# Optimization experiments

Hardware: AMD Instinct MI355X
Metric: run time of the kernel (lower is better)

The kernel has to match this reference:

```python
import jax, jax.numpy as jnp
import numpy as np

B, NW, WS, FD = 16, 256, 8, 96
D = WS * WS * FD        # 6144 flattened window dim
MID = 512               # expert hidden dim
NE = 16                 # num experts


def setup_inputs() -> dict:
    key = jax.random.key(0)
    ks = jax.random.split(key, 7)
    s1 = 1.0 / np.sqrt(D)
    s2 = 1.0 / np.sqrt(MID)
    x = jax.random.normal(ks[0], (B, NW, WS, WS, FD), dtype=jnp.float32)
    # stacked expert weights (torch Linear: y = x @ W.T + b)
    w1 = jax.random.uniform(ks[1], (NE, D, MID), jnp.float32, -s1, s1)
    b1 = jax.random.uniform(ks[2], (NE, MID), jnp.float32, -s1, s1)
    w2 = jax.random.uniform(ks[3], (NE, MID), jnp.float32, -s2, s2)  # out dim 1, squeezed
    b2 = jax.random.uniform(ks[4], (NE,), jnp.float32, -s2, s2)
    gw = jax.random.uniform(ks[5], (D, NE), jnp.float32, -s1, s1)
    gb = jax.random.uniform(ks[6], (NE,), jnp.float32, -s1, s1)
    return {"x": x, "w1": w1, "b1": b1, "w2": w2, "b2": b2, "gw": gw, "gb": gb}


def reference(x, w1, b1, w2, b2, gw, gb):
    bsz, nw = x.shape[0], x.shape[1]
    xf = x.reshape(bsz * nw, D)                          # [T, D]
    h = jax.nn.relu(jnp.einsum('td,ndm->tnm', xf, w1) + b1)  # [T, N, MID]
    e = jnp.einsum('tnm,nm->tn', h, w2) + b2             # [T, N] expert scalar outputs
    g = jax.nn.softmax(xf @ gw + gb, axis=-1)            # [T, N] gating
    out = jax.nn.sigmoid(jnp.sum(g * e, axis=-1))        # [T]
    return out.reshape(bsz, nw)
```

## Files before the change

### kernel.cpp

```cpp
#include <hip/hip_runtime.h>
#include <hip/hip_bf16.h>
#include <stdint.h>

#define T_TOK 4096
#define DD    6144
#define MIDD  512
#define NEXP  16

typedef __attribute__((ext_vector_type(8))) __bf16 bf16x8;
typedef __attribute__((ext_vector_type(4))) float  f32x4;

__device__ __forceinline__ unsigned short f2bf(float f) {
  unsigned int u = __builtin_bit_cast(unsigned int, f);
  u += 0x7fffu + ((u >> 16) & 1u);
  return (unsigned short)(u >> 16);
}

__device__ __forceinline__ void gload16(const void* g, void* l) {
  __builtin_amdgcn_global_load_lds((__attribute__((address_space(1))) void*)g,
                                   (__attribute__((address_space(3))) void*)l,
                                   16, 0, 0);
}

__global__ __launch_bounds__(256) void k_cvt_x(const float4* __restrict__ x,
                                               ushort4* __restrict__ xb, int n4) {
  int i = blockIdx.x * blockDim.x + threadIdx.x;
  const int stride = gridDim.x * blockDim.x;
  for (; i < n4; i += stride) {
    const float4 v = x[i];
    ushort4 o;
    o.x = f2bf(v.x); o.y = f2bf(v.y); o.z = f2bf(v.z); o.w = f2bf(v.w);
    xb[i] = o;
  }
}

__global__ __launch_bounds__(256) void k_trc_w1(const float* __restrict__ w1,
                                                unsigned short* __restrict__ w1t) {
  __shared__ float tile[32][33];
  const int n  = blockIdx.z;
  const int d0 = blockIdx.y * 32;
  const int m0 = blockIdx.x * 32;
  const int r  = threadIdx.x >> 3;
  const int c4 = threadIdx.x & 7;

  const float4 v = *(const float4*)(w1 + (size_t)n * DD * MIDD +
                                    (size_t)(d0 + r) * MIDD + m0 + c4 * 4);
  tile[r][c4 * 4 + 0] = v.x;
  tile[r][c4 * 4 + 1] = v.y;
  tile[r][c4 * 4 + 2] = v.z;
  tile[r][c4 * 4 + 3] = v.w;
  __syncthreads();
  ushort4 o;
  o.x = f2bf(tile[c4 * 4 + 0][r]);
  o.y = f2bf(tile[c4 * 4 + 1][r]);
  o.z = f2bf(tile[c4 * 4 + 2][r]);
  o.w = f2bf(tile[c4 * 4 + 3][r]);
  *(ushort4*)(w1t + (size_t)n * MIDD * DD + (size_t)(m0 + r) * DD + d0 + c4 * 4) = o;
}

__global__ __launch_bounds__(256) void k_gemm(const unsigned short* __restrict__ Xb,
                                              const unsigned short* __restrict__ W1T,
                                              const float* __restrict__ b1,
                                              const float* __restrict__ w2,
                                              float* __restrict__ e_part) {
  __shared__ char lds[16384];
  char* ldsA = lds;
  char* ldsB = lds + 8192;

  const int tid  = threadIdx.x;
  const int wid  = tid >> 6;
  const int lane = tid & 63;
  const int bn   = blockIdx.x;
  const int bm   = blockIdx.y;
  const int row0 = bm * 128;
  const int col0 = bn * 128;
  const int ne   = col0 >> 9;
  const int m0   = col0 & 511;
  const int wr = wid >> 1, wc = wid & 1;
  const int kb = lane >> 4, lr = lane & 15;

  f32x4 acc[4][4] = {};

  const unsigned short* Ag = Xb + (size_t)row0 * DD + wid * 8;
  const unsigned short* Bg = W1T + ((size_t)ne * MIDD + m0) * DD + wid * 8;
  char* ldsAw = ldsA + wid * 2048;
  char* ldsBw = ldsB + wid * 2048;

  for (int k0 = 0; k0 < DD; k0 += 32) {
    __syncthreads();
    gload16(Ag + (size_t)lane        * DD + k0, ldsAw);
    gload16(Ag + (size_t)(64 + lane) * DD + k0, ldsAw + 1024);
    gload16(Bg + (size_t)lane        * DD + k0, ldsBw);
    gload16(Bg + (size_t)(64 + lane) * DD + k0, ldsBw + 1024);
    __syncthreads();

    bf16x8 af[4], bfr[4];
#pragma unroll
    for (int m = 0; m < 4; ++m)
      af[m] = *(const bf16x8*)(ldsA + kb * 2048 + (wr * 64 + m * 16 + lr) * 16);
#pragma unroll
    for (int nn = 0; nn < 4; ++nn)
      bfr[nn] = *(const bf16x8*)(ldsB + kb * 2048 + (wc * 64 + nn * 16 + lr) * 16);
#pragma unroll
    for (int m = 0; m < 4; ++m)
#pragma unroll
      for (int nn = 0; nn < 4; ++nn)
        acc[m][nn] = __builtin_amdgcn_mfma_f32_16x16x32_bf16(af[m], bfr[nn],
                                                             acc[m][nn], 0, 0, 0);
  }

  const int part = ((bn & 3) << 1) | wc;
  float b1v[4], w2v[4];
#pragma unroll
  for (int bj = 0; bj < 4; ++bj) {
    const int mcol = m0 + wc * 64 + bj * 16 + lr;
    b1v[bj] = b1[ne * MIDD + mcol];
    w2v[bj] = w2[ne * MIDD + mcol];
  }
#pragma unroll
  for (int ai = 0; ai < 4; ++ai) {
#pragma unroll
    for (int i = 0; i < 4; ++i) {
      float s = 0.f;
#pragma unroll
      for (int bj = 0; bj < 4; ++bj) {
        float h = acc[ai][bj][i] + b1v[bj];
        h = fmaxf(h, 0.f);
        s += h * w2v[bj];
      }
      s += __shfl_xor(s, 1);
      s += __shfl_xor(s, 2);
      s += __shfl_xor(s, 4);
      s += __shfl_xor(s, 8);
      if (lr == 0) {
        const int row = row0 + wr * 64 + ai * 16 + kb * 4 + i;
        e_part[((size_t)row * NEXP + ne) * 8 + part] = s;
      }
    }
  }
}

__global__ __launch_bounds__(256) void k_gate(const float* __restrict__ x,
                                              const float* __restrict__ gw,
                                              float* __restrict__ l_part) {
  const int tl = threadIdx.x >> 2, ng = threadIdx.x & 3;
  const int tg = blockIdx.x >> 3, ds = blockIdx.x & 7;
  const int t  = tg * 64 + tl;
  const float* xp  = x  + (size_t)t * DD + ds * 768;
  const float* gwp = gw + (size_t)(ds * 768) * NEXP + ng * 4;
  float a[4] = {0.f, 0.f, 0.f, 0.f};
  for (int c = 0; c < 768; c += 4) {
    const float4 xv = *(const float4*)(xp + c);
    const float xs[4] = {xv.x, xv.y, xv.z, xv.w};
#pragma unroll
    for (int j = 0; j < 4; ++j) {
      const float4 g4 = *(const float4*)(gwp + (size_t)(c + j) * NEXP);
      a[0] += xs[j] * g4.x; a[1] += xs[j] * g4.y;
      a[2] += xs[j] * g4.z; a[3] += xs[j] * g4.w;
    }
  }
  float* lp = l_part + ((size_t)t * NEXP + ng * 4) * 8 + ds;
  lp[0] = a[0]; lp[8] = a[1]; lp[16] = a[2]; lp[24] = a[3];
}

__global__ __launch_bounds__(256) void k_combine(const float* __restrict__ l_part,
                                                 const float* __restrict__ e_part,
                                                 const float* __restrict__ gb,
                                                 const float* __restrict__ b2,
                                                 float* __restrict__ out) {
  const int tl = threadIdx.x >> 4, n = threadIdx.x & 15;
  const int t  = blockIdx.x * 16 + tl;
  const float4* lp = (const float4*)(l_part + ((size_t)t * NEXP + n) * 8);
  const float4 l0 = lp[0], l1 = lp[1];
  const float logit = l0.x + l0.y + l0.z + l0.w + l1.x + l1.y + l1.z + l1.w + gb[n];
  const float4* ep = (const float4*)(e_part + ((size_t)t * NEXP + n) * 8);
  const float4 e0 = ep[0], e1 = ep[1];
  const float ev = e0.x + e0.y + e0.z + e0.w + e1.x + e1.y + e1.z + e1.w + b2[n];
  float m = logit;
  m = fmaxf(m, __shfl_xor(m, 1));
  m = fmaxf(m, __shfl_xor(m, 2));
  m = fmaxf(m, __shfl_xor(m, 4));
  m = fmaxf(m, __shfl_xor(m, 8));
  const float p = __expf(logit - m);
  float pe = p * ev, pz = p;
  pe += __shfl_xor(pe, 1); pz += __shfl_xor(pz, 1);
  pe += __shfl_xor(pe, 2); pz += __shfl_xor(pz, 2);
  pe += __shfl_xor(pe, 4); pz += __shfl_xor(pz, 4);
  pe += __shfl_xor(pe, 8); pz += __shfl_xor(pz, 8);
  if (n == 0) {
    const float z = pe / pz;
    out[t] = 1.f / (1.f + __expf(-z));
  }
}

extern "C" void kernel_launch(void* const* d_in, const int* in_sizes, int n_in,
                              void* d_out, int out_size, void* d_ws, size_t ws_size,
                              hipStream_t stream) {
  const float* x  = (const float*)d_in[0];
  const float* w1 = (const float*)d_in[1];
  const float* b1 = (const float*)d_in[2];
  const float* w2 = (const float*)d_in[3];
  const float* b2 = (const float*)d_in[4];
  const float* gw = (const float*)d_in[5];
  const float* gb = (const float*)d_in[6];
  float* out = (float*)d_out;

  char* ws = (char*)d_ws;
  unsigned short* Xb  = (unsigned short*)ws;
  unsigned short* W1T = (unsigned short*)(ws + 50331648);
  float* e_part = (float*)(ws + 150994944);
  float* l_part = (float*)(ws + 153092096);

  k_cvt_x<<<2048, 256, 0, stream>>>((const float4*)x, (ushort4*)Xb, (T_TOK * DD) / 4);
  k_trc_w1<<<dim3(MIDD / 32, DD / 32, NEXP), 256, 0, stream>>>(w1, W1T);
  k_gemm<<<dim3(64, 32), 256, 0, stream>>>(Xb, W1T, b1, w2, e_part);
  k_gate<<<512, 256, 0, stream>>>(x, gw, l_part);
  k_combine<<<256, 256, 0, stream>>>(l_part, e_part, gb, b2, out);
}
```

Measured before the change: 1.227 ms.

## Double-buffer GEMM LDS loads, remap blocks for XCD locality, widen w1 transpose tiles

The GEMM now double-buffers its A/B tiles in LDS, issuing the next k-slice's global-to-LDS loads before the current slice's MFMAs, which cuts one barrier per iteration. The grid becomes 1D with an index remap that interleaves blocks (blockIdx&7 shifted high) so blocks likely co-resident on the same chiplet share row/column tiles in cache. The w1 transpose kernel moves to 64x64 tiles with 16-byte stores to improve write coalescing. The cost is doubled LDS per block (32 KB), which may lower occupancy, and a more complex block mapping.

```diff
diff --git a/kernel.cpp b/kernel.cpp
--- a/kernel.cpp
+++ b/kernel.cpp
@@ -9,6 +9,7 @@
 
 typedef __attribute__((ext_vector_type(8))) __bf16 bf16x8;
 typedef __attribute__((ext_vector_type(4))) float  f32x4;
+typedef __attribute__((ext_vector_type(8))) unsigned short ushort8_t;
 
 __device__ __forceinline__ unsigned short f2bf(float f) {
   unsigned int u = __builtin_bit_cast(unsigned int, f);
@@ -36,26 +37,35 @@
 
 __global__ __launch_bounds__(256) void k_trc_w1(const float* __restrict__ w1,
                                                 unsigned short* __restrict__ w1t) {
-  __shared__ float tile[32][33];
+  __shared__ float tile[64][65];
+  const int tid = threadIdx.x;
   const int n  = blockIdx.z;
-  const int d0 = blockIdx.y * 32;
-  const int m0 = blockIdx.x * 32;
-  const int r  = threadIdx.x >> 3;
-  const int c4 = threadIdx.x & 7;
-
-  const float4 v = *(const float4*)(w1 + (size_t)n * DD * MIDD +
-                                    (size_t)(d0 + r) * MIDD + m0 + c4 * 4);
-  tile[r][c4 * 4 + 0] = v.x;
-  tile[r][c4 * 4 + 1] = v.y;
-  tile[r][c4 * 4 + 2] = v.z;
-  tile[r][c4 * 4 + 3] = v.w;
+  const int d0 = blockIdx.y * 64;
+  const int m0 = blockIdx.x * 64;
+
+  const int rr = tid >> 4;
+  const int c4 = tid & 15;
+  const float* src = w1 + (size_t)n * DD * MIDD + (size_t)d0 * MIDD + m0;
+#pragma unroll
+  for (int r = 0; r < 4; ++r) {
+    const int row = rr + 16 * r;
+    const float4 v = *(const float4*)(src + (size_t)row * MIDD + c4 * 4);
+    tile[row][c4 * 4 + 0] = v.x;
+    tile[row][c4 * 4 + 1] = v.y;
+    tile[row][c4 * 4 + 2] = v.z;
+    tile[row][c4 * 4 + 3] = v.w;
+  }
   __syncthreads();
-  ushort4 o;
-  o.x = f2bf(tile[c4 * 4 + 0][r]);
-  o.y = f2bf(tile[c4 * 4 + 1][r]);
-  o.z = f2bf(tile[c4 * 4 + 2][r]);
-  o.w = f2bf(tile[c4 * 4 + 3][r]);
-  *(ushort4*)(w1t + (size_t)n * MIDD * DD + (size_t)(m0 + r) * DD + d0 + c4 * 4) = o;
+  unsigned short* dst = w1t + (size_t)n * MIDD * DD + (size_t)m0 * DD + d0;
+  const int dc = tid & 7;
+#pragma unroll
+  for (int wrr = 0; wrr < 2; ++wrr) {
+    const int m = (tid >> 3) + 32 * wrr;
+    ushort8_t o;
+#pragma unroll
+    for (int j = 0; j < 8; ++j) o[j] = f2bf(tile[dc * 8 + j][m]);
+    *(ushort8_t*)(dst + (size_t)m * DD + dc * 8) = o;
+  }
 }
 
 __global__ __launch_bounds__(256) void k_gemm(const unsigned short* __restrict__ Xb,
@@ -63,15 +73,14 @@
                                               const float* __restrict__ b1,
                                               const float* __restrict__ w2,
                                               float* __restrict__ e_part) {
-  __shared__ char lds[16384];
-  char* ldsA = lds;
-  char* ldsB = lds + 8192;
+  __shared__ char lds[32768];
 
   const int tid  = threadIdx.x;
   const int wid  = tid >> 6;
   const int lane = tid & 63;
-  const int bn   = blockIdx.x;
-  const int bm   = blockIdx.y;
+  const int wq = ((blockIdx.x & 7) << 8) | ((int)blockIdx.x >> 3);
+  const int bm = wq & 31;
+  const int bn = ((wq >> 8) << 3) | ((wq >> 5) & 7);
   const int row0 = bm * 128;
   const int col0 = bn * 128;
   const int ne   = col0 >> 9;
@@ -83,17 +92,34 @@
 
   const unsigned short* Ag = Xb + (size_t)row0 * DD + wid * 8;
   const unsigned short* Bg = W1T + ((size_t)ne * MIDD + m0) * DD + wid * 8;
-  char* ldsAw = ldsA + wid * 2048;
-  char* ldsBw = ldsB + wid * 2048;
-
+  const unsigned short* a0 = Ag + (size_t)lane * DD;
+  const unsigned short* a1 = Ag + (size_t)(64 + lane) * DD;
+  const unsigned short* b0 = Bg + (size_t)lane * DD;
+  const unsigned short* b1g = Bg + (size_t)(64 + lane) * DD;
+
+  {
+    char* ldsAw = lds + wid * 2048;
+    char* ldsBw = lds + 8192 + wid * 2048;
+    gload16(a0, ldsAw);
+    gload16(a1, ldsAw + 1024);
+    gload16(b0, ldsBw);
+    gload16(b1g, ldsBw + 1024);
+  }
+  __syncthreads();
+
+  int cur = 0;
   for (int k0 = 0; k0 < DD; k0 += 32) {
-    __syncthreads();
-    gload16(Ag + (size_t)lane        * DD + k0, ldsAw);
-    gload16(Ag + (size_t)(64 + lane) * DD + k0, ldsAw + 1024);
-    gload16(Bg + (size_t)lane        * DD + k0, ldsBw);
-    gload16(Bg + (size_t)(64 + lane) * DD + k0, ldsBw + 1024);
-    __syncthreads();
-
+    if (k0 + 32 < DD) {
+      char* ldsAw = lds + (cur ^ 1) * 16384 + wid * 2048;
+      char* ldsBw = lds + (cur ^ 1) * 16384 + 8192 + wid * 2048;
+      const int kn = k0 + 32;
+      gload16(a0 + kn, ldsAw);
+      gload16(a1 + kn, ldsAw + 1024);
+      gload16(b0 + kn, ldsBw);
+      gload16(b1g + kn, ldsBw + 1024);
+    }
+    const char* ldsA = lds + cur * 16384;
+    const char* ldsB = ldsA + 8192;
     bf16x8 af[4], bfr[4];
 #pragma unroll
     for (int m = 0; m < 4; ++m)
@@ -107,6 +133,8 @@
       for (int nn = 0; nn < 4; ++nn)
         acc[m][nn] = __builtin_amdgcn_mfma_f32_16x16x32_bf16(af[m], bfr[nn],
                                                              acc[m][nn], 0, 0, 0);
+    __syncthreads();
+    cur ^= 1;
   }
 
   const int part = ((bn & 3) << 1) | wc;
@@ -212,8 +240,8 @@
   float* l_part = (float*)(ws + 153092096);
 
   k_cvt_x<<<2048, 256, 0, stream>>>((const float4*)x, (ushort4*)Xb, (T_TOK * DD) / 4);
-  k_trc_w1<<<dim3(MIDD / 32, DD / 32, NEXP), 256, 0, stream>>>(w1, W1T);
-  k_gemm<<<dim3(64, 32), 256, 0, stream>>>(Xb, W1T, b1, w2, e_part);
+  k_trc_w1<<<dim3(MIDD / 64, DD / 64, NEXP), 256, 0, stream>>>(w1, W1T);
+  k_gemm<<<2048, 256, 0, stream>>>(Xb, W1T, b1, w2, e_part);
   k_gate<<<512, 256, 0, stream>>>(x, gw, l_part);
   k_combine<<<256, 256, 0, stream>>>(l_part, e_part, gb, b2, out);
 }
```

Result: slower. 1.282 ms (+4.4%).
